# Kernel optimization log

Hardware: AMD Instinct MI355X
Metric: run time of the kernel (lower is better)

Reference implementation:

```python
import jax, jax.numpy as jnp
import numpy as np

S, B, D = 1024, 2, 1024      # seq, batch, embed_dim
E, TOPK = 15, 3              # routed experts = 8*2-1, top_n = 2*2-1
F = 1024                     # per-expert ffn dim (ffn_dim // m)
FS = 2048                    # shared expert ffn dim (ffn_dim * n_shared)


def _uinit(k, shape, out_dim):
    std = out_dim ** -0.5
    return jax.random.uniform(k, shape, jnp.float32, -std, std)


def setup_inputs() -> dict:
    key = jax.random.key(0)
    ks = jax.random.split(key, 10)
    return {
        "x": jax.random.normal(ks[0], (S, B, D), jnp.float32),
        "gate_w": jax.random.normal(ks[1], (E, D), jnp.float32) * (D ** -0.5),
        "fc1_w": _uinit(ks[2], (E, 2 * F, D), 2 * F),
        "fc1_b": _uinit(ks[3], (E, 2 * F), 2 * F),
        "geglu_mult": jnp.ones((E, F), jnp.float32),
        "fc2_w": _uinit(ks[4], (E, D, F), D),
        "fc2_b": _uinit(ks[5], (E, D), D),
        "s_fc1_w": _uinit(ks[6], (2 * FS, D), 2 * FS),
        "s_fc1_b": _uinit(ks[7], (2 * FS,), 2 * FS),
        "s_geglu_mult": jnp.ones((FS,), jnp.float32),
        "s_fc2_w": _uinit(ks[8], (D, FS), D),
        "s_fc2_b": _uinit(ks[9], (D,), D),
    }


def reference(x, gate_w, fc1_w, fc1_b, geglu_mult, fc2_w, fc2_b,
              s_fc1_w, s_fc1_b, s_geglu_mult, s_fc2_w, s_fc2_b):
    s, b, d = x.shape
    xt = x.reshape(-1, d)                              # [T, D] tokens
    T = xt.shape[0]

    # --- gate: softmax over routed experts, top-k, renormalize ---
    logits = xt @ gate_w.T                             # [T, E]
    scores = jax.nn.softmax(logits, axis=-1)
    topk_w, topk_idx = jax.lax.top_k(scores, TOPK)     # [T, K]
    topk_w = topk_w / (jnp.sum(topk_w, axis=-1, keepdims=True) + 1e-20)
    # combine weights: zero for non-routed experts (same math as dispatch/scatter)
    comb = jnp.zeros((T, E), xt.dtype).at[jnp.arange(T)[:, None], topk_idx].add(topk_w)

    # --- routed experts: GEGLU FFN applied as grouped GEMM, weighted combine ---
    h = jnp.einsum('td,efd->etf', xt, fc1_w) + fc1_b[:, None, :]   # [E, T, 2F]
    xh, g = h[..., :F], h[..., F:]                                 # chunk: (x, gate)
    a = jax.nn.gelu(g, approximate=False) * xh * geglu_mult[:, None, :]
    yexp = jnp.einsum('etf,edf->etd', a, fc2_w) + fc2_b[:, None, :]  # [E, T, D]
    y = jnp.einsum('etd,te->td', yexp, comb)                         # [T, D]

    # --- shared expert ---
    hs = xt @ s_fc1_w.T + s_fc1_b                      # [T, 2*FS]
    xs, gs = hs[..., :FS], hs[..., FS:]
    as_ = jax.nn.gelu(gs, approximate=False) * xs * s_geglu_mult
    ys = as_ @ s_fc2_w.T + s_fc2_b                     # [T, D]

    return (y + ys).reshape(s, b, d)
```

## Files before the change

kernel.cpp:

```cpp
#include <hip/hip_runtime.h>

typedef __attribute__((ext_vector_type(8))) short bfrag;
typedef __attribute__((ext_vector_type(4))) float f32x4;

__device__ __forceinline__ short f2bf(float f) {
  union { float f; unsigned u; } v; v.f = f;
  unsigned r = v.u + 0x7FFFu + ((v.u >> 16) & 1u);
  return (short)(r >> 16);
}
__device__ __forceinline__ float bf2f(unsigned short h) {
  union { unsigned u; float f; } v; v.u = ((unsigned)h) << 16;
  return v.f;
}
__device__ __forceinline__ float gelu_exact(float g) {
  return 0.5f * g * (1.0f + erff(g * 0.70710678118654752f));
}
__device__ __forceinline__ void gld_lds16(const short* g, short* l) {
  __builtin_amdgcn_global_load_lds(
      (const __attribute__((address_space(1))) void*)g,
      (__attribute__((address_space(3))) void*)l, 16, 0, 0);
}

__global__ __launch_bounds__(256) void k_convert_w(
    const float* __restrict__ s0, const float* __restrict__ s1,
    const float* __restrict__ s2, const float* __restrict__ s3,
    short* __restrict__ d0, short* __restrict__ d1,
    short* __restrict__ d2, short* __restrict__ d3)
{
  const int b = blockIdx.x;
  const float* s; short* d; long off;
  if (b < 15360)      { s = s0; d = d0; off = (long)b * 512; }
  else if (b < 23040) { s = s1; d = d1; off = (long)(b - 15360) * 512; }
  else if (b < 25088) { s = s2; d = d2; off = (long)(b - 23040) * 512; }
  else                { s = s3; d = d3; off = (long)(b - 25088) * 512; }
  const long i = off + threadIdx.x;
  const float4 va = ((const float4*)s)[i];
  const float4 vb = ((const float4*)s)[i + 256];
  ((short4*)d)[i]       = make_short4(f2bf(va.x), f2bf(va.y), f2bf(va.z), f2bf(va.w));
  ((short4*)d)[i + 256] = make_short4(f2bf(vb.x), f2bf(vb.y), f2bf(vb.z), f2bf(vb.w));
}

__global__ __launch_bounds__(64) void k_gate(const float* __restrict__ x,
    const float* __restrict__ gw, int* __restrict__ topk_idx,
    float* __restrict__ topk_w, short* __restrict__ xbf)
{
  const int t0 = blockIdx.x * 4;
  const int lane = threadIdx.x;
  float xv[4][16];
#pragma unroll
  for (int tt = 0; tt < 4; tt++)
#pragma unroll
    for (int i = 0; i < 16; i++) {
      xv[tt][i] = x[(size_t)(t0 + tt) * 1024 + lane + 64 * i];
      xbf[(size_t)(t0 + tt) * 1024 + lane + 64 * i] = f2bf(xv[tt][i]);
    }
  float p[4][15];
#pragma unroll
  for (int e = 0; e < 15; e++) {
    float wv[16];
#pragma unroll
    for (int i = 0; i < 16; i++) wv[i] = gw[(size_t)e * 1024 + lane + 64 * i];
#pragma unroll
    for (int tt = 0; tt < 4; tt++) {
      float s = 0.f;
#pragma unroll
      for (int i = 0; i < 16; i++) s += xv[tt][i] * wv[i];
#pragma unroll
      for (int o = 32; o; o >>= 1) s += __shfl_xor(s, o, 64);
      p[tt][e] = s;
    }
  }
#pragma unroll
  for (int tt = 0; tt < 4; tt++) {
    float m = -1e30f;
#pragma unroll
    for (int e = 0; e < 15; e++) m = fmaxf(m, p[tt][e]);
    float q[15], Z = 0.f;
#pragma unroll
    for (int e = 0; e < 15; e++) { q[e] = expf(p[tt][e] - m); Z += q[e]; }
    int usedMask = 0; int bi[3]; float bv[3];
#pragma unroll
    for (int j = 0; j < 3; j++) {
      float best = -1.f; int b = 0;
#pragma unroll
      for (int e = 0; e < 15; e++) {
        bool ok = (!((usedMask >> e) & 1)) && (q[e] > best);
        if (ok) { best = q[e]; b = e; }
      }
      bi[j] = b; bv[j] = best / Z; usedMask |= 1 << b;
    }
    if (lane == tt) {
      float den = bv[0] + bv[1] + bv[2] + 1e-20f;
#pragma unroll
      for (int j = 0; j < 3; j++) {
        topk_idx[(t0 + tt) * 3 + j] = bi[j];
        topk_w[(t0 + tt) * 3 + j] = bv[j] / den;
      }
    }
  }
}

__global__ __launch_bounds__(1024) void k_route(const int* __restrict__ topk_idx,
    const float* __restrict__ topk_w, int* __restrict__ cnt_g, int* __restrict__ offs_g,
    int* __restrict__ row_tok, float* __restrict__ row_wt, int* __restrict__ row_id)
{
  __shared__ int scnt[16], soffs[16], sfill[16];
  const int tid = threadIdx.x;
  if (tid < 16) { scnt[tid] = 0; sfill[tid] = 0; }
  __syncthreads();
  for (int i = tid; i < 6144; i += 1024) atomicAdd(&scnt[topk_idx[i]], 1);
  __syncthreads();
  if (tid == 0) {
    int a = 0;
    for (int e = 0; e < 15; e++) { soffs[e] = a; offs_g[e] = a; cnt_g[e] = scnt[e]; a += scnt[e]; }
  }
  __syncthreads();
  for (int i = tid; i < 6144; i += 1024) {
    int e = topk_idx[i];
    int pos = atomicAdd(&sfill[e], 1);
    int row = soffs[e] + pos;
    row_tok[row] = i / 3;
    row_wt[row] = topk_w[i];
    row_id[i] = row;
  }
}

__device__ __forceinline__ bool resolve_tile128(const int* __restrict__ cnt, int ty,
                                                int& e, int& lt) {
  int acc = 0;
#pragma unroll
  for (int i = 0; i < 15; i++) {
    int tl = (cnt[i] + 127) >> 7;
    if (ty < acc + tl) { e = i; lt = ty - acc; return true; }
    acc += tl;
  }
  return false;
}

__global__ __launch_bounds__(256) void k_fc1(
    const short* __restrict__ xbf,
    const short* __restrict__ wsh, const float* __restrict__ bsh, const float* __restrict__ msh,
    const short* __restrict__ wex, const float* __restrict__ bex, const float* __restrict__ mex,
    const int* __restrict__ cnt, const int* __restrict__ offs, const int* __restrict__ row_tok,
    short* __restrict__ as_buf, short* __restrict__ a_buf)
{
  __shared__ short smem[4 * 128 * 64];
  const int tid = threadIdx.x;
  const int bid = blockIdx.x;
  const bool sh = bid < 512;
  int f0, m0 = 0, e = 0, rowBase = 0, nrows = 128;
  if (sh) {
    f0 = (bid & 31) * 64; m0 = (bid >> 5) * 128;
  } else {
    const int b2 = bid - 512;
    int lt;
    if (!resolve_tile128(cnt, b2 >> 4, e, lt)) return;
    f0 = (b2 & 15) * 64;
    rowBase = offs[e] + lt * 128;
    nrows = cnt[e] - lt * 128; if (nrows > 128) nrows = 128;
  }
  const int lane = tid & 63, ml = lane & 15, kq = lane >> 4, mlo = lane & 7;
  const int wv = tid >> 6, wr = wv >> 1, wc = wv & 1;
  const int lrow = lane >> 3, lchk = lane & 7;
  const int Fhalf = sh ? 2048 : 1024;
  const short* wptr = sh ? wsh : (wex + (size_t)e * 2048 * 1024);
  const short* aSrc[4]; const short* bSrc[4];
#pragma unroll
  for (int t = 0; t < 4; t++) {
    const int r = wv * 32 + t * 8 + lrow;
    const int sc = (lchk ^ (r & 7)) * 8;
    if (sh) aSrc[t] = xbf + (size_t)(m0 + r) * 1024 + sc;
    else {
      const int rc = r < nrows ? r : nrows - 1;
      aSrc[t] = xbf + (size_t)row_tok[rowBase + rc] * 1024 + sc;
    }
    const int grow = (r < 64) ? (f0 + r) : (Fhalf + f0 + r - 64);
    bSrc[t] = wptr + (size_t)grow * 1024 + sc;
  }
  f32x4 acc[4][4] = {};

#define FC1_STAGE(BUF, K0) do {                                              \
    short* A_ = smem + (BUF) * 16384;                                        \
    short* B_ = A_ + 8192;                                                   \
    _Pragma("unroll")                                                        \
    for (int t = 0; t < 4; t++) gld_lds16(aSrc[t] + (K0), A_ + (wv * 32 + t * 8) * 64); \
    _Pragma("unroll")                                                        \
    for (int t = 0; t < 4; t++) gld_lds16(bSrc[t] + (K0), B_ + (wv * 32 + t * 8) * 64); \
  } while (0)

#define FC1_COMPUTE(BUF) do {                                                \
    const short* As_ = smem + (BUF) * 16384;                                 \
    const short* Bs_ = As_ + 8192;                                           \
    _Pragma("unroll")                                                        \
    for (int kk = 0; kk < 2; kk++) {                                         \
      const int so = ((kk * 4 + kq) ^ mlo) * 8;                              \
      bfrag af[4], bb[4];                                                    \
      _Pragma("unroll")                                                      \
      for (int i = 0; i < 4; i++)                                            \
        af[i] = *(const bfrag*)&As_[(wr * 64 + i * 16 + ml) * 64 + so];      \
      _Pragma("unroll")                                                      \
      for (int j = 0; j < 4; j++) {                                          \
        const int brow = ((j >> 1) ? 64 : 0) + wc * 32 + (j & 1) * 16 + ml;  \
        bb[j] = *(const bfrag*)&Bs_[brow * 64 + so];                         \
      }                                                                      \
      _Pragma("unroll")                                                      \
      for (int i = 0; i < 4; i++)                                            \
        _Pragma("unroll")                                                    \
        for (int j = 0; j < 4; j++)                                          \
          acc[i][j] = __builtin_amdgcn_mfma_f32_16x16x32_bf16(af[i], bb[j], acc[i][j], 0, 0, 0); \
    }                                                                        \
  } while (0)

  FC1_STAGE(0, 0);
  __syncthreads();
  int cur = 0;
  for (int ks = 0; ks < 15; ks++) {
    FC1_STAGE(cur ^ 1, (ks + 1) * 64);
    FC1_COMPUTE(cur);
    __syncthreads();
    cur ^= 1;
  }
  FC1_COMPUTE(cur);

  const float* bias = sh ? bsh : (bex + (size_t)e * 2048);
  const float* mult = sh ? msh : (mex + (size_t)e * 1024);
#pragma unroll
  for (int jj = 0; jj < 2; jj++) {
    const int fl = wc * 32 + jj * 16 + ml;
    const int f = f0 + fl;
    const float b1 = bias[f];
    const float b2 = bias[Fhalf + f];
    const float mv = mult[f];
#pragma unroll
    for (int i = 0; i < 4; i++)
#pragma unroll
      for (int rg = 0; rg < 4; rg++) {
        const int row = wr * 64 + i * 16 + kq * 4 + rg;
        const float h1 = acc[i][jj][rg] + b1;
        const float h2 = acc[i][jj + 2][rg] + b2;
        const short o = f2bf(gelu_exact(h2) * h1 * mv);
        if (sh) as_buf[(size_t)(m0 + row) * 2048 + f] = o;
        else if (row < nrows) a_buf[(size_t)(rowBase + row) * 1024 + f] = o;
      }
  }
}

__global__ __launch_bounds__(256) void k_fc2(
    const short* __restrict__ as_buf, const short* __restrict__ wsfc2, const float* __restrict__ s_b,
    const short* __restrict__ a_buf, const short* __restrict__ wfc2, const float* __restrict__ e_b,
    const int* __restrict__ cnt, const int* __restrict__ offs, const float* __restrict__ row_wt,
    float* __restrict__ y, short* __restrict__ yexp)
{
  __shared__ short smem[4 * 128 * 64];
  const int tid = threadIdx.x;
  const int bid = blockIdx.x;
  const bool sh = bid < 128;
  int d0, m0 = 0, e = 0, rowBase = 0, nrows = 128, Klen, astr, bstr;
  const short *aBase, *bBase;
  if (sh) {
    d0 = (bid & 7) * 128; m0 = (bid >> 3) * 128;
    Klen = 2048; astr = 2048; bstr = 2048;
    aBase = as_buf; bBase = wsfc2;
  } else {
    const int b2 = bid - 128;
    int lt;
    if (!resolve_tile128(cnt, b2 >> 3, e, lt)) return;
    d0 = (b2 & 7) * 128;
    rowBase = offs[e] + lt * 128;
    nrows = cnt[e] - lt * 128; if (nrows > 128) nrows = 128;
    Klen = 1024; astr = 1024; bstr = 1024;
    aBase = a_buf + (size_t)rowBase * 1024;
    bBase = wfc2 + (size_t)e * 1024 * 1024;
  }
  const int lane = tid & 63, ml = lane & 15, kq = lane >> 4, mlo = lane & 7;
  const int wv = tid >> 6, wr = wv >> 1, wc = wv & 1;
  const int lrow = lane >> 3, lchk = lane & 7;
  const short* aSrc[4]; const short* bSrc[4];
#pragma unroll
  for (int t = 0; t < 4; t++) {
    const int r = wv * 32 + t * 8 + lrow;
    const int sc = (lchk ^ (r & 7)) * 8;
    aSrc[t] = aBase + (size_t)(sh ? (m0 + r) : r) * astr + sc;
    bSrc[t] = bBase + (size_t)(d0 + r) * bstr + sc;
  }
  f32x4 acc[4][4] = {};

#define FC2_STAGE(BUF, K0) do {                                              \
    short* A_ = smem + (BUF) * 16384;                                        \
    short* B_ = A_ + 8192;                                                   \
    _Pragma("unroll")                                                        \
    for (int t = 0; t < 4; t++) gld_lds16(aSrc[t] + (K0), A_ + (wv * 32 + t * 8) * 64); \
    _Pragma("unroll")                                                        \
    for (int t = 0; t < 4; t++) gld_lds16(bSrc[t] + (K0), B_ + (wv * 32 + t * 8) * 64); \
  } while (0)

#define FC2_COMPUTE(BUF) do {                                                \
    const short* As_ = smem + (BUF) * 16384;                                 \
    const short* Bs_ = As_ + 8192;                                           \
    _Pragma("unroll")                                                        \
    for (int kk = 0; kk < 2; kk++) {                                         \
      const int so = ((kk * 4 + kq) ^ mlo) * 8;                              \
      bfrag af[4], bb[4];                                                    \
      _Pragma("unroll")                                                      \
      for (int i = 0; i < 4; i++)                                            \
        af[i] = *(const bfrag*)&As_[(wr * 64 + i * 16 + ml) * 64 + so];      \
      _Pragma("unroll")                                                      \
      for (int j = 0; j < 4; j++)                                            \
        bb[j] = *(const bfrag*)&Bs_[(wc * 64 + j * 16 + ml) * 64 + so];      \
      _Pragma("unroll")                                                      \
      for (int i = 0; i < 4; i++)                                            \
        _Pragma("unroll")                                                    \
        for (int j = 0; j < 4; j++)                                          \
          acc[i][j] = __builtin_amdgcn_mfma_f32_16x16x32_bf16(af[i], bb[j], acc[i][j], 0, 0, 0); \
    }                                                                        \
  } while (0)

  FC2_STAGE(0, 0);
  __syncthreads();
  int cur = 0;
  const int NK = Klen >> 6;
  for (int ks = 0; ks < NK - 1; ks++) {
    FC2_STAGE(cur ^ 1, (ks + 1) * 64);
    FC2_COMPUTE(cur);
    __syncthreads();
    cur ^= 1;
  }
  FC2_COMPUTE(cur);

#pragma unroll
  for (int j = 0; j < 4; j++) {
    const int d = d0 + wc * 64 + j * 16 + ml;
    const float bv = sh ? s_b[d] : e_b[(size_t)e * 1024 + d];
#pragma unroll
    for (int i = 0; i < 4; i++)
#pragma unroll
      for (int rg = 0; rg < 4; rg++) {
        const int row = wr * 64 + i * 16 + kq * 4 + rg;
        if (sh) {
          y[(size_t)(m0 + row) * 1024 + d] = acc[i][j][rg] + bv;
        } else if (row < nrows) {
          const float wt = row_wt[rowBase + row];
          yexp[(size_t)(rowBase + row) * 1024 + d] = f2bf((acc[i][j][rg] + bv) * wt);
        }
      }
  }
}

__global__ __launch_bounds__(256) void k_combine(float* __restrict__ y,
    const short* __restrict__ yexp, const int* __restrict__ row_id)
{
  const int idx = blockIdx.x * 256 + threadIdx.x;
  const int t = idx >> 8;
  const int d4 = (idx & 255) * 4;
  const int r0 = row_id[t * 3], r1 = row_id[t * 3 + 1], r2 = row_id[t * 3 + 2];
  float4 acc = *(float4*)(y + (size_t)t * 1024 + d4);
  const ushort4 v0 = *(const ushort4*)(yexp + (size_t)r0 * 1024 + d4);
  const ushort4 v1 = *(const ushort4*)(yexp + (size_t)r1 * 1024 + d4);
  const ushort4 v2 = *(const ushort4*)(yexp + (size_t)r2 * 1024 + d4);
  acc.x += bf2f(v0.x) + bf2f(v1.x) + bf2f(v2.x);
  acc.y += bf2f(v0.y) + bf2f(v1.y) + bf2f(v2.y);
  acc.z += bf2f(v0.z) + bf2f(v1.z) + bf2f(v2.z);
  acc.w += bf2f(v0.w) + bf2f(v1.w) + bf2f(v2.w);
  *(float4*)(y + (size_t)t * 1024 + d4) = acc;
}

extern "C" void kernel_launch(void* const* d_in, const int* in_sizes, int n_in,
                              void* d_out, int out_size, void* d_ws, size_t ws_size,
                              hipStream_t stream) {
  const float* x          = (const float*)d_in[0];
  const float* gate_w     = (const float*)d_in[1];
  const float* fc1_w      = (const float*)d_in[2];
  const float* fc1_b      = (const float*)d_in[3];
  const float* geglu_mult = (const float*)d_in[4];
  const float* fc2_w      = (const float*)d_in[5];
  const float* fc2_b      = (const float*)d_in[6];
  const float* s_fc1_w    = (const float*)d_in[7];
  const float* s_fc1_b    = (const float*)d_in[8];
  const float* s_mult     = (const float*)d_in[9];
  const float* s_fc2_w    = (const float*)d_in[10];
  const float* s_fc2_b    = (const float*)d_in[11];
  float* y = (float*)d_out;

  char* wsb = (char*)d_ws;
  int*   cnt      = (int*)(wsb + 0);
  int*   offs     = (int*)(wsb + 64);
  int*   topk_idx = (int*)(wsb + 256);
  float* topk_w   = (float*)(wsb + 24832);
  int*   row_tok  = (int*)(wsb + 49408);
  float* row_wt   = (float*)(wsb + 74496);
  int*   row_id   = (int*)(wsb + 99584);
  short* xbf      = (short*)(wsb + 131072);
  short* a_buf    = (short*)(wsb + 8519680);
  short* as_buf   = (short*)(wsb + 21364736);
  short* yexp     = (short*)(wsb + 29753344);
  short* wbf_sfc1 = (short*)(wsb + 42598400);
  short* wbf_sfc2 = (short*)(wsb + 50987008);
  short* wbf_fc1  = (short*)(wsb + 55181312);
  short* wbf_fc2  = (short*)(wsb + 118095872);

  k_convert_w<<<26112, 256, 0, stream>>>(fc1_w, fc2_w, s_fc1_w, s_fc2_w,
                                         wbf_fc1, wbf_fc2, wbf_sfc1, wbf_sfc2);
  k_gate<<<512, 64, 0, stream>>>(x, gate_w, topk_idx, topk_w, xbf);
  k_route<<<1, 1024, 0, stream>>>(topk_idx, topk_w, cnt, offs, row_tok, row_wt, row_id);
  k_fc1<<<1520, 256, 0, stream>>>(xbf, wbf_sfc1, s_fc1_b, s_mult,
                                  wbf_fc1, fc1_b, geglu_mult,
                                  cnt, offs, row_tok, as_buf, a_buf);
  k_fc2<<<632, 256, 0, stream>>>(as_buf, wbf_sfc2, s_fc2_b,
                                 a_buf, wbf_fc2, fc2_b,
                                 cnt, offs, row_wt, y, yexp);
  k_combine<<<2048, 256, 0, stream>>>(y, yexp, row_id);
}
```

Baseline: 434.8 us.

## Fuse fp32-to-bf16 weight conversion into GEMM B-tile loading

Removes the standalone weight conversion kernel. The fc1 and fc2 GEMMs now read fp32 weights straight into registers, pack them to bf16 with v_cvt_pk_bf16_f32, and write them to LDS. The existing swizzle is kept by reading the swizzled source column into a linear LDS slot. This avoids the large write and re-read of the bf16 weight copy. In exchange, each GEMM tile fetches twice the weight bytes from global memory, repeated across M tiles, and the B loads go through registers instead of the async direct-to-LDS path, which adds register pressure and VALU work inside the main loop.

```diff
diff --git a/kernel.cpp b/kernel.cpp
--- a/kernel.cpp
+++ b/kernel.cpp
@@ -12,6 +12,11 @@
   union { unsigned u; float f; } v; v.u = ((unsigned)h) << 16;
   return v.f;
 }
+__device__ __forceinline__ unsigned cvtpk(float lo, float hi) {
+  unsigned r;
+  asm("v_cvt_pk_bf16_f32 %0, %1, %2" : "=v"(r) : "v"(lo), "v"(hi));
+  return r;
+}
 __device__ __forceinline__ float gelu_exact(float g) {
   return 0.5f * g * (1.0f + erff(g * 0.70710678118654752f));
 }
@@ -19,25 +24,6 @@
   __builtin_amdgcn_global_load_lds(
       (const __attribute__((address_space(1))) void*)g,
       (__attribute__((address_space(3))) void*)l, 16, 0, 0);
-}
-
-__global__ __launch_bounds__(256) void k_convert_w(
-    const float* __restrict__ s0, const float* __restrict__ s1,
-    const float* __restrict__ s2, const float* __restrict__ s3,
-    short* __restrict__ d0, short* __restrict__ d1,
-    short* __restrict__ d2, short* __restrict__ d3)
-{
-  const int b = blockIdx.x;
-  const float* s; short* d; long off;
-  if (b < 15360)      { s = s0; d = d0; off = (long)b * 512; }
-  else if (b < 23040) { s = s1; d = d1; off = (long)(b - 15360) * 512; }
-  else if (b < 25088) { s = s2; d = d2; off = (long)(b - 23040) * 512; }
-  else                { s = s3; d = d3; off = (long)(b - 25088) * 512; }
-  const long i = off + threadIdx.x;
-  const float4 va = ((const float4*)s)[i];
-  const float4 vb = ((const float4*)s)[i + 256];
-  ((short4*)d)[i]       = make_short4(f2bf(va.x), f2bf(va.y), f2bf(va.z), f2bf(va.w));
-  ((short4*)d)[i + 256] = make_short4(f2bf(vb.x), f2bf(vb.y), f2bf(vb.z), f2bf(vb.w));
 }
 
 __global__ __launch_bounds__(64) void k_gate(const float* __restrict__ x,
@@ -139,8 +125,8 @@
 
 __global__ __launch_bounds__(256) void k_fc1(
     const short* __restrict__ xbf,
-    const short* __restrict__ wsh, const float* __restrict__ bsh, const float* __restrict__ msh,
-    const short* __restrict__ wex, const float* __restrict__ bex, const float* __restrict__ mex,
+    const float* __restrict__ wsh, const float* __restrict__ bsh, const float* __restrict__ msh,
+    const float* __restrict__ wex, const float* __restrict__ bex, const float* __restrict__ mex,
     const int* __restrict__ cnt, const int* __restrict__ offs, const int* __restrict__ row_tok,
     short* __restrict__ as_buf, short* __restrict__ a_buf)
 {
@@ -163,8 +149,9 @@
   const int wv = tid >> 6, wr = wv >> 1, wc = wv & 1;
   const int lrow = lane >> 3, lchk = lane & 7;
   const int Fhalf = sh ? 2048 : 1024;
-  const short* wptr = sh ? wsh : (wex + (size_t)e * 2048 * 1024);
-  const short* aSrc[4]; const short* bSrc[4];
+  const float* wptr = sh ? wsh : (wex + (size_t)e * 2048 * 1024);
+  const short* aSrc[4]; const float* bSrc[4];
+  const int bDst = lchk * 8;
 #pragma unroll
   for (int t = 0; t < 4; t++) {
     const int r = wv * 32 + t * 8 + lrow;
@@ -178,14 +165,33 @@
     bSrc[t] = wptr + (size_t)grow * 1024 + sc;
   }
   f32x4 acc[4][4] = {};
-
-#define FC1_STAGE(BUF, K0) do {                                              \
+  float4 br[8];
+
+#define FC1_A_STAGE(BUF, K0) do {                                            \
     short* A_ = smem + (BUF) * 16384;                                        \
-    short* B_ = A_ + 8192;                                                   \
     _Pragma("unroll")                                                        \
     for (int t = 0; t < 4; t++) gld_lds16(aSrc[t] + (K0), A_ + (wv * 32 + t * 8) * 64); \
-    _Pragma("unroll")                                                        \
-    for (int t = 0; t < 4; t++) gld_lds16(bSrc[t] + (K0), B_ + (wv * 32 + t * 8) * 64); \
+  } while (0)
+
+#define FC1_B_LOAD(K0) do {                                                  \
+    _Pragma("unroll")                                                        \
+    for (int t = 0; t < 4; t++) {                                            \
+      br[2 * t]     = *(const float4*)(bSrc[t] + (K0));                      \
+      br[2 * t + 1] = *(const float4*)(bSrc[t] + (K0) + 4);                  \
+    }                                                                        \
+  } while (0)
+
+#define FC1_B_WRITE(BUF) do {                                                \
+    short* B_ = smem + (BUF) * 16384 + 8192;                                 \
+    _Pragma("unroll")                                                        \
+    for (int t = 0; t < 4; t++) {                                            \
+      int4 w;                                                                \
+      w.x = cvtpk(br[2 * t].x, br[2 * t].y);                                 \
+      w.y = cvtpk(br[2 * t].z, br[2 * t].w);                                 \
+      w.z = cvtpk(br[2 * t + 1].x, br[2 * t + 1].y);                         \
+      w.w = cvtpk(br[2 * t + 1].z, br[2 * t + 1].w);                         \
+      *(int4*)&B_[(wv * 32 + t * 8 + lrow) * 64 + bDst] = w;                 \
+    }                                                                        \
   } while (0)
 
 #define FC1_COMPUTE(BUF) do {                                                \
@@ -211,12 +217,16 @@
     }                                                                        \
   } while (0)
 
-  FC1_STAGE(0, 0);
+  FC1_A_STAGE(0, 0);
+  FC1_B_LOAD(0);
+  FC1_B_WRITE(0);
   __syncthreads();
   int cur = 0;
   for (int ks = 0; ks < 15; ks++) {
-    FC1_STAGE(cur ^ 1, (ks + 1) * 64);
+    FC1_A_STAGE(cur ^ 1, (ks + 1) * 64);
+    FC1_B_LOAD((ks + 1) * 64);
     FC1_COMPUTE(cur);
+    FC1_B_WRITE(cur ^ 1);
     __syncthreads();
     cur ^= 1;
   }
@@ -246,8 +256,8 @@
 }
 
 __global__ __launch_bounds__(256) void k_fc2(
-    const short* __restrict__ as_buf, const short* __restrict__ wsfc2, const float* __restrict__ s_b,
-    const short* __restrict__ a_buf, const short* __restrict__ wfc2, const float* __restrict__ e_b,
+    const short* __restrict__ as_buf, const float* __restrict__ wsfc2, const float* __restrict__ s_b,
+    const short* __restrict__ a_buf, const float* __restrict__ wfc2, const float* __restrict__ e_b,
     const int* __restrict__ cnt, const int* __restrict__ offs, const float* __restrict__ row_wt,
     float* __restrict__ y, short* __restrict__ yexp)
 {
@@ -256,7 +266,7 @@
   const int bid = blockIdx.x;
   const bool sh = bid < 128;
   int d0, m0 = 0, e = 0, rowBase = 0, nrows = 128, Klen, astr, bstr;
-  const short *aBase, *bBase;
+  const short* aBase; const float* bBase;
   if (sh) {
     d0 = (bid & 7) * 128; m0 = (bid >> 3) * 128;
     Klen = 2048; astr = 2048; bstr = 2048;
@@ -275,7 +285,8 @@
   const int lane = tid & 63, ml = lane & 15, kq = lane >> 4, mlo = lane & 7;
   const int wv = tid >> 6, wr = wv >> 1, wc = wv & 1;
   const int lrow = lane >> 3, lchk = lane & 7;
-  const short* aSrc[4]; const short* bSrc[4];
+  const int bDst = lchk * 8;
+  const short* aSrc[4]; const float* bSrc[4];
 #pragma unroll
   for (int t = 0; t < 4; t++) {
     const int r = wv * 32 + t * 8 + lrow;
@@ -284,14 +295,33 @@
     bSrc[t] = bBase + (size_t)(d0 + r) * bstr + sc;
   }
   f32x4 acc[4][4] = {};
-
-#define FC2_STAGE(BUF, K0) do {                                              \
+  float4 br[8];
+
+#define FC2_A_STAGE(BUF, K0) do {                                            \
     short* A_ = smem + (BUF) * 16384;                                        \
-    short* B_ = A_ + 8192;                                                   \
     _Pragma("unroll")                                                        \
     for (int t = 0; t < 4; t++) gld_lds16(aSrc[t] + (K0), A_ + (wv * 32 + t * 8) * 64); \
-    _Pragma("unroll")                                                        \
-    for (int t = 0; t < 4; t++) gld_lds16(bSrc[t] + (K0), B_ + (wv * 32 + t * 8) * 64); \
+  } while (0)
+
+#define FC2_B_LOAD(K0) do {                                                  \
+    _Pragma("unroll")                                                        \
+    for (int t = 0; t < 4; t++) {                                            \
+      br[2 * t]     = *(const float4*)(bSrc[t] + (K0));                      \
+      br[2 * t + 1] = *(const float4*)(bSrc[t] + (K0) + 4);                  \
+    }                                                                        \
+  } while (0)
+
+#define FC2_B_WRITE(BUF) do {                                                \
+    short* B_ = smem + (BUF) * 16384 + 8192;                                 \
+    _Pragma("unroll")                                                        \
+    for (int t = 0; t < 4; t++) {                                            \
+      int4 w;                                                                \
+      w.x = cvtpk(br[2 * t].x, br[2 * t].y);                                 \
+      w.y = cvtpk(br[2 * t].z, br[2 * t].w);                                 \
+      w.z = cvtpk(br[2 * t + 1].x, br[2 * t + 1].y);                         \
+      w.w = cvtpk(br[2 * t + 1].z, br[2 * t + 1].w);                         \
+      *(int4*)&B_[(wv * 32 + t * 8 + lrow) * 64 + bDst] = w;                 \
+    }                                                                        \
   } while (0)
 
 #define FC2_COMPUTE(BUF) do {                                                \
@@ -315,13 +345,17 @@
     }                                                                        \
   } while (0)
 
-  FC2_STAGE(0, 0);
+  FC2_A_STAGE(0, 0);
+  FC2_B_LOAD(0);
+  FC2_B_WRITE(0);
   __syncthreads();
   int cur = 0;
   const int NK = Klen >> 6;
   for (int ks = 0; ks < NK - 1; ks++) {
-    FC2_STAGE(cur ^ 1, (ks + 1) * 64);
+    FC2_A_STAGE(cur ^ 1, (ks + 1) * 64);
+    FC2_B_LOAD((ks + 1) * 64);
     FC2_COMPUTE(cur);
+    FC2_B_WRITE(cur ^ 1);
     __syncthreads();
     cur ^= 1;
   }
@@ -393,20 +427,14 @@
   short* a_buf    = (short*)(wsb + 8519680);
   short* as_buf   = (short*)(wsb + 21364736);
   short* yexp     = (short*)(wsb + 29753344);
-  short* wbf_sfc1 = (short*)(wsb + 42598400);
-  short* wbf_sfc2 = (short*)(wsb + 50987008);
-  short* wbf_fc1  = (short*)(wsb + 55181312);
-  short* wbf_fc2  = (short*)(wsb + 118095872);
-
-  k_convert_w<<<26112, 256, 0, stream>>>(fc1_w, fc2_w, s_fc1_w, s_fc2_w,
-                                         wbf_fc1, wbf_fc2, wbf_sfc1, wbf_sfc2);
+
   k_gate<<<512, 64, 0, stream>>>(x, gate_w, topk_idx, topk_w, xbf);
   k_route<<<1, 1024, 0, stream>>>(topk_idx, topk_w, cnt, offs, row_tok, row_wt, row_id);
-  k_fc1<<<1520, 256, 0, stream>>>(xbf, wbf_sfc1, s_fc1_b, s_mult,
-                                  wbf_fc1, fc1_b, geglu_mult,
+  k_fc1<<<1520, 256, 0, stream>>>(xbf, s_fc1_w, s_fc1_b, s_mult,
+                                  fc1_w, fc1_b, geglu_mult,
                                   cnt, offs, row_tok, as_buf, a_buf);
-  k_fc2<<<632, 256, 0, stream>>>(as_buf, wbf_sfc2, s_fc2_b,
-                                 a_buf, wbf_fc2, fc2_b,
+  k_fc2<<<632, 256, 0, stream>>>(as_buf, s_fc2_w, s_fc2_b,
+                                 a_buf, fc2_w, fc2_b,
                                  cnt, offs, row_wt, y, yexp);
   k_combine<<<2048, 256, 0, stream>>>(y, yexp, row_id);
 }
```

New measurement: 479.4 us. +10.3%, slower.
